# Performance work log

Measured on AMD Instinct MI355X. Metric: run time of the kernel, lower is better.

The kernel has to match this reference:

```python
import jax, jax.numpy as jnp
import numpy as np

B, K, C = 512, 64, 2048  # batch, mixture components, copy (eval points)


def setup_inputs() -> dict:
    key = jax.random.key(0)
    kw, km, ks, kr, kx = jax.random.split(key, 5)
    w = jax.random.uniform(kw, (B, K), dtype=jnp.float32)            # mixture weights
    means = jax.random.normal(km, (B, K, 2), dtype=jnp.float32)      # mean1, mean2
    sds = jax.random.uniform(ks, (B, K, 2), dtype=jnp.float32,
                             minval=0.5, maxval=1.5)                 # sd1, sd2 (>0)
    corr = jax.random.uniform(kr, (B, K), dtype=jnp.float32,
                              minval=-0.8, maxval=0.8)               # |corr| < 1
    model_out = jnp.concatenate(
        [w[..., None], means, sds, corr[..., None]], axis=-1)        # [B, K, 6]
    X = jax.random.normal(kx, (B, C, 2), dtype=jnp.float32)
    return {"model_out": model_out, "X": X}


def reference(model_out, X):
    # Unpack params: w, mean1, mean2, sd1, sd2, corr  -- each [B, K]
    w = model_out[..., 0]
    m1 = model_out[..., 1]
    m2 = model_out[..., 2]
    s1 = model_out[..., 3]
    s2 = model_out[..., 4]
    r = model_out[..., 5]

    # Closed-form bivariate normal pdf (equivalent to Cholesky-based
    # MultivariateNormal log_prob for the 2x2 covariance built in torch).
    # dx, dy: [B, C, K] via broadcasting X[B,C,1] against params[B,1,K]
    dx = (X[:, :, 0:1] - m1[:, None, :]) / s1[:, None, :]
    dy = (X[:, :, 1:2] - m2[:, None, :]) / s2[:, None, :]
    rb = r[:, None, :]
    omr2 = 1.0 - rb * rb  # 1 - rho^2
    z = dx * dx - 2.0 * rb * dx * dy + dy * dy
    two_pi = 2.0 * jnp.pi
    norm = two_pi * s1[:, None, :] * s2[:, None, :] * jnp.sqrt(omr2)
    probs = jnp.exp(-0.5 * z / omr2) / norm  # [B, C, K]

    # Weighted sum over components -> [B, C]
    return jnp.einsum('bck,bk->bc', probs, w)
```

## Files before the change

### kernel.cpp

```cpp
#include <hip/hip_runtime.h>
#include <hip/hip_bf16.h>


constexpr int B = 512;
constexpr int K = 64;
constexpr int C = 2048;
constexpr int BLOCK = 256;

__global__ __launch_bounds__(BLOCK) void mixture_kernel(
    const float* __restrict__ mo,
    const float* __restrict__ X,
    float* __restrict__ out)
{
    __shared__ float4 P[K][2];

    const int b = blockIdx.x;
    const int t = threadIdx.x;

    if (t < K) {
        const float* p = mo + ((size_t)(b * K + t)) * 6;
        const float w  = p[0];
        const float m1 = p[1];
        const float m2 = p[2];
        const float s1 = p[3];
        const float s2 = p[4];
        const float r  = p[5];

        const float omr2 = fmaf(-r, r, 1.0f);
        const float inv  = 1.0f / omr2;
        const float a2   = 0.7213475204444817f * inv;
        const float sc   = sqrtf(a2);
        const float is1  = sc / s1;
        const float is2  = sc / s2;
        const float wn   = w * 0.15915494309189535f / (s1 * s2 * sqrtf(omr2));

        P[t][0] = make_float4(is1, is2, m1 * is1, m2 * is2);
        P[t][1] = make_float4(2.0f * r, wn, 0.0f, 0.0f);
    }
    __syncthreads();

    const float4* Xb = (const float4*)(X + (size_t)b * C * 2);
    float4 xv[4];
#pragma unroll
    for (int j = 0; j < 4; ++j) xv[j] = Xb[t + j * BLOCK];

    float acc[8];
#pragma unroll
    for (int i = 0; i < 8; ++i) acc[i] = 0.0f;

    for (int k = 0; k < K; ++k) {
        const float4 p0 = P[k][0];
        const float4 p1 = P[k][1];
#pragma unroll
        for (int j = 0; j < 4; ++j) {
            const float dx0 = fmaf(xv[j].x, p0.x, -p0.z);
            const float dy0 = fmaf(xv[j].y, p0.y, -p0.w);
            const float dx1 = fmaf(xv[j].z, p0.x, -p0.z);
            const float dy1 = fmaf(xv[j].w, p0.y, -p0.w);
            const float q0  = fmaf(dy0, dy0, dx0 * dx0);
            const float q1  = fmaf(dy1, dy1, dx1 * dx1);
            const float e0  = fmaf(p1.x, dx0 * dy0, -q0);
            const float e1  = fmaf(p1.x, dx1 * dy1, -q1);
            acc[2 * j]     = fmaf(p1.y, __builtin_amdgcn_exp2f(e0), acc[2 * j]);
            acc[2 * j + 1] = fmaf(p1.y, __builtin_amdgcn_exp2f(e1), acc[2 * j + 1]);
        }
    }

    float2* ob = (float2*)(out + (size_t)b * C);
#pragma unroll
    for (int j = 0; j < 4; ++j)
        ob[t + j * BLOCK] = make_float2(acc[2 * j], acc[2 * j + 1]);
}

extern "C" void kernel_launch(void* const* d_in, const int* in_sizes, int n_in,
                              void* d_out, int out_size, void* d_ws, size_t ws_size,
                              hipStream_t stream) {
    const float* mo = (const float*)d_in[0];
    const float* X  = (const float*)d_in[1];
    float* out      = (float*)d_out;

    mixture_kernel<<<dim3(B), dim3(BLOCK), 0, stream>>>(mo, X, out);
}
```

Before: 77.04 us.

## Split each batch across two blocks and use packed float2 FMA math

Launches two blocks per batch row, each covering half of the eval points, so the grid doubles to give more waves across the CUs. The inner math moves to two-wide vector types so the compiler can emit packed FP32 FMA/MUL instructions, and the k loop is unrolled by 4 with a launch-bounds occupancy hint. In exchange, each block recomputes the per-component parameter table, which doubles that setup work, and each thread now handles fewer points, which gives less ILP per thread.

```diff
diff --git a/kernel.cpp b/kernel.cpp
--- a/kernel.cpp
+++ b/kernel.cpp
@@ -1,21 +1,27 @@
 #include <hip/hip_runtime.h>
 #include <hip/hip_bf16.h>
 
+
+typedef float v2f __attribute__((ext_vector_type(2)));
 
 constexpr int B = 512;
 constexpr int K = 64;
 constexpr int C = 2048;
 constexpr int BLOCK = 256;
+constexpr int HALVES = 2;
+constexpr int CH = C / HALVES;
 
-__global__ __launch_bounds__(BLOCK) void mixture_kernel(
+__global__ __launch_bounds__(BLOCK, 4) void mixture_kernel(
     const float* __restrict__ mo,
     const float* __restrict__ X,
     float* __restrict__ out)
 {
     __shared__ float4 P[K][2];
 
-    const int b = blockIdx.x;
-    const int t = threadIdx.x;
+    const int bid = blockIdx.x;
+    const int b   = bid >> 1;
+    const int h   = bid & 1;
+    const int t   = threadIdx.x;
 
     if (t < K) {
         const float* p = mo + ((size_t)(b * K + t)) * 6;
@@ -39,37 +45,42 @@
     }
     __syncthreads();
 
-    const float4* Xb = (const float4*)(X + (size_t)b * C * 2);
-    float4 xv[4];
-#pragma unroll
-    for (int j = 0; j < 4; ++j) xv[j] = Xb[t + j * BLOCK];
+    const float4* Xb = (const float4*)(X + (size_t)b * C * 2 + (size_t)h * CH * 2);
+    const float4 xv0 = Xb[t];
+    const float4 xv1 = Xb[t + BLOCK];
 
-    float acc[8];
-#pragma unroll
-    for (int i = 0; i < 8; ++i) acc[i] = 0.0f;
+    v2f xs[2] = { {xv0.x, xv0.z}, {xv1.x, xv1.z} };
+    v2f ys[2] = { {xv0.y, xv0.w}, {xv1.y, xv1.w} };
+    v2f acc[2] = { {0.0f, 0.0f}, {0.0f, 0.0f} };
 
+#pragma unroll 4
     for (int k = 0; k < K; ++k) {
         const float4 p0 = P[k][0];
         const float4 p1 = P[k][1];
+        const v2f vis1 = { p0.x, p0.x };
+        const v2f vis2 = { p0.y, p0.y };
+        const v2f vnm1 = { -p0.z, -p0.z };
+        const v2f vnm2 = { -p0.w, -p0.w };
+        const v2f v2r  = { p1.x, p1.x };
+        const v2f vwn  = { p1.y, p1.y };
 #pragma unroll
-        for (int j = 0; j < 4; ++j) {
-            const float dx0 = fmaf(xv[j].x, p0.x, -p0.z);
-            const float dy0 = fmaf(xv[j].y, p0.y, -p0.w);
-            const float dx1 = fmaf(xv[j].z, p0.x, -p0.z);
-            const float dy1 = fmaf(xv[j].w, p0.y, -p0.w);
-            const float q0  = fmaf(dy0, dy0, dx0 * dx0);
-            const float q1  = fmaf(dy1, dy1, dx1 * dx1);
-            const float e0  = fmaf(p1.x, dx0 * dy0, -q0);
-            const float e1  = fmaf(p1.x, dx1 * dy1, -q1);
-            acc[2 * j]     = fmaf(p1.y, __builtin_amdgcn_exp2f(e0), acc[2 * j]);
-            acc[2 * j + 1] = fmaf(p1.y, __builtin_amdgcn_exp2f(e1), acc[2 * j + 1]);
+        for (int j = 0; j < 2; ++j) {
+            const v2f dx = __builtin_elementwise_fma(xs[j], vis1, vnm1);
+            const v2f dy = __builtin_elementwise_fma(ys[j], vis2, vnm2);
+            const v2f pq = dx * dy;
+            v2f u        = dx * dx;
+            u            = __builtin_elementwise_fma(dy, dy, u);
+            const v2f e  = __builtin_elementwise_fma(v2r, pq, -u);
+            v2f ex;
+            ex.x = __builtin_amdgcn_exp2f(e.x);
+            ex.y = __builtin_amdgcn_exp2f(e.y);
+            acc[j] = __builtin_elementwise_fma(vwn, ex, acc[j]);
         }
     }
 
-    float2* ob = (float2*)(out + (size_t)b * C);
-#pragma unroll
-    for (int j = 0; j < 4; ++j)
-        ob[t + j * BLOCK] = make_float2(acc[2 * j], acc[2 * j + 1]);
+    float2* ob = (float2*)(out + (size_t)b * C + (size_t)h * CH);
+    ob[t]         = make_float2(acc[0].x, acc[0].y);
+    ob[t + BLOCK] = make_float2(acc[1].x, acc[1].y);
 }
 
 extern "C" void kernel_launch(void* const* d_in, const int* in_sizes, int n_in,
@@ -79,5 +90,5 @@
     const float* X  = (const float*)d_in[1];
     float* out      = (float*)d_out;
 
-    mixture_kernel<<<dim3(B), dim3(BLOCK), 0, stream>>>(mo, X, out);
+    mixture_kernel<<<dim3(B * HALVES), dim3(BLOCK), 0, stream>>>(mo, X, out);
 }
```

After: 72.35 us. 1.06x faster.
